# Kernel optimization log

Measured on AMD Instinct MI355X. Metric: run time of the kernel, lower is better.

Reference implementation:

```python
import jax, jax.numpy as jnp
import numpy as np

B, C, H, W = 4, 64, 64, 64

def setup_inputs() -> dict:
    key = jax.random.key(0)
    ks = jax.random.split(key, 7)
    s = 1.0 / np.sqrt(C)
    return {
        "x": jax.random.normal(ks[0], (B, C, H, W), dtype=jnp.float32),
        "Wq": jax.random.normal(ks[1], (C, C), dtype=jnp.float32) * s,
        "bq": jax.random.normal(ks[2], (C,), dtype=jnp.float32) * s,
        "Wk": jax.random.normal(ks[3], (C, C), dtype=jnp.float32) * s,
        "bk": jax.random.normal(ks[4], (C,), dtype=jnp.float32) * s,
        "Wv": jax.random.normal(ks[5], (C, C), dtype=jnp.float32) * s,
        "bv": jax.random.normal(ks[6], (C,), dtype=jnp.float32) * s,
    }

def reference(x, Wq, bq, Wk, bk, Wv, bv):
    b, c, h, w = x.shape
    n = h * w
    xf = x.reshape(b, c, n)                                   # (B,C,N)
    # 1x1 convs == per-pixel linear maps over channels
    q = jnp.einsum('oc,bcn->bon', Wq, xf) + bq[None, :, None]  # (B,C,N)
    k = jnp.einsum('oc,bcn->bon', Wk, xf) + bk[None, :, None]  # (B,C,N)
    v = jnp.einsum('oc,bcn->bon', Wv, xf) + bv[None, :, None]  # (B,C,N)
    # energy = Q^T K : (B,N,N); note: no 1/sqrt(C) scaling in the original
    energy = jnp.einsum('bcn,bcm->bnm', q, k)
    attention = jax.nn.softmax(energy, axis=-1)
    # out = V @ attention^T : out[:, :, i] = sum_j V[:, :, j] * attention[i, j]
    out = jnp.einsum('bcm,bnm->bcn', v, attention)
    return out.reshape(b, c, h, w)
```

## Files before the change

### kernel.cpp

```cpp
#include <hip/hip_runtime.h>
#include <math.h>

#define T_N 4096
#define T_C 64
#define T_B 4
#define NSLICE 4
#define TILES_PER_SLICE (64 / NSLICE)

typedef __attribute__((ext_vector_type(8))) _Float16 f16x8;
typedef __attribute__((ext_vector_type(4))) _Float16 f16x4;
typedef __attribute__((ext_vector_type(4))) float f32x4;

__device__ inline unsigned short f2h(float f) {
    union { _Float16 h; unsigned short s; } u; u.h = (_Float16)f; return u.s;
}
__device__ inline float h2f(unsigned short s) {
    union { unsigned short s; _Float16 h; } u; u.s = s; return (float)u.h;
}

__global__ __launch_bounds__(256) void qkv_kernel(
    const float* __restrict__ x,
    const float* __restrict__ Wq, const float* __restrict__ bq,
    const float* __restrict__ Wk, const float* __restrict__ bk,
    const float* __restrict__ Wv, const float* __restrict__ bv,
    unsigned short* __restrict__ qt, unsigned short* __restrict__ kt,
    unsigned short* __restrict__ vb)
{
    __shared__ __align__(16) unsigned short xsh[32 * 72];
    __shared__ __align__(16) unsigned short xsl[32 * 72];
    __shared__ __align__(16) unsigned short wf[3][64 * 72];

    const int tid = threadIdx.x;
    const int n0  = blockIdx.x * 32;
    const int b   = blockIdx.y;
    const float* xb = x + (size_t)b * T_C * T_N;

    const float* Ws[3] = {Wq, Wk, Wv};
    #pragma unroll
    for (int p = 0; p < 3; ++p) {
        for (int i = tid; i < 1024; i += 256) {
            const int o = i >> 4, c4 = (i & 15) * 4;
            const float4 w4 = ((const float4*)Ws[p])[i];
            f16x4 wh;
            wh[0] = (_Float16)w4.x; wh[1] = (_Float16)w4.y;
            wh[2] = (_Float16)w4.z; wh[3] = (_Float16)w4.w;
            *(f16x4*)&wf[p][o * 72 + c4] = wh;
        }
    }
    for (int i = tid; i < 512; i += 256) {
        const int c = i >> 3, nj4 = (i & 7) * 4;
        const float4 xv = *(const float4*)&xb[c * T_N + n0 + nj4];
        const float xa[4] = {xv.x, xv.y, xv.z, xv.w};
        #pragma unroll
        for (int j = 0; j < 4; ++j) {
            const unsigned short h = f2h(xa[j]);
            xsh[(nj4 + j) * 72 + c] = h;
            xsl[(nj4 + j) * 72 + c] = f2h(xa[j] - h2f(h));
        }
    }
    __syncthreads();

    const int wv_  = tid >> 6;
    const int lane = tid & 63;
    const int quad = lane >> 4;
    const int col  = lane & 15;
    const int pst  = (wv_ & 1) * 16;
    const int oh   = (wv_ >> 1) * 2;
    const size_t bN = (size_t)b * T_N;

    f16x8 xh[2], xl[2];
    #pragma unroll
    for (int s = 0; s < 2; ++s) {
        xh[s] = *(const f16x8*)&xsh[(pst + col) * 72 + s * 32 + quad * 8];
        xl[s] = *(const f16x8*)&xsl[(pst + col) * 72 + s * 32 + quad * 8];
    }
    __syncthreads();

    const float* biases[3] = {bq, bk, bv};
    for (int p = 0; p < 3; ++p) {
        #pragma unroll
        for (int oo = 0; oo < 2; ++oo) {
            const int osub = oh + oo;
            f32x4 acc = (f32x4){0.f, 0.f, 0.f, 0.f};
            #pragma unroll
            for (int s = 0; s < 2; ++s) {
                const f16x8 wfr =
                    *(const f16x8*)&wf[p][(osub * 16 + col) * 72 + s * 32 + quad * 8];
                acc = __builtin_amdgcn_mfma_f32_16x16x32_f16(xh[s], wfr, acc, 0, 0, 0);
                acc = __builtin_amdgcn_mfma_f32_16x16x32_f16(xl[s], wfr, acc, 0, 0, 0);
            }
            const float bb = biases[p][osub * 16 + col];
            if (p < 2) {
                #pragma unroll
                for (int r = 0; r < 4; ++r)
                    xsh[(pst + quad * 4 + r) * 72 + osub * 16 + col] = f2h(acc[r] + bb);
            } else {
                union { ushort4 v; unsigned short s[4]; } hv;
                #pragma unroll
                for (int r = 0; r < 4; ++r) hv.s[r] = f2h(acc[r] + bb);
                *(ushort4*)&xsh[(osub * 16 + col) * 36 + pst + quad * 4] = hv.v;
            }
        }
        __syncthreads();
        if (p < 2) {
            const int pix = tid >> 3, c8 = (tid & 7) * 8;
            unsigned short* dst = (p == 0) ? qt : kt;
            *(f16x8*)&dst[(bN + n0 + pix) * 64 + c8] = *(const f16x8*)&xsh[pix * 72 + c8];
            __syncthreads();
        } else {
            const int o = tid >> 2, p8 = (tid & 3) * 8;
            *(f16x8*)&vb[((size_t)(b * 64 + o)) * T_N + n0 + p8] =
                *(const f16x8*)&xsh[o * 36 + p8];
        }
    }
}

__global__ __launch_bounds__(256, 4) void attn_kernel(
    const unsigned short* __restrict__ qt,
    const unsigned short* __restrict__ kt, const unsigned short* __restrict__ vb,
    unsigned short* __restrict__ o_part, float* __restrict__ mp, float* __restrict__ lp)
{
    __shared__ __align__(16) unsigned short ks[64 * 64];
    __shared__ __align__(16) unsigned short vs[64 * 64];

    const int tid   = threadIdx.x;
    const int n0    = blockIdx.x * 64;
    const int slice = blockIdx.y;
    const int b     = blockIdx.z;
    const int wv_   = tid >> 6;
    const int lane  = tid & 63;
    const int quad  = lane >> 4;
    const int col   = lane & 15;

    const size_t bN = (size_t)b * T_N;
    const int q_own = n0 + wv_ * 16 + col;

    f16x8 qh[2];
    #pragma unroll
    for (int s = 0; s < 2; ++s)
        qh[s] = *(const f16x8*)&qt[(bN + q_own) * 64 + s * 32 + quad * 8];

    const int row = tid >> 3, cc = tid & 7;
    const int pc  = (cc ^ (row & 7)) * 8;

    const int mbase = slice * TILES_PER_SLICE * 64;
    float4 p0, p1, p2, p3;
    p0 = *(const float4*)&kt[(bN + mbase + row) * 64 + cc * 8];
    p1 = *(const float4*)&kt[(bN + mbase + 32 + row) * 64 + cc * 8];
    p2 = *(const float4*)&vb[((size_t)(b * 64 + row)) * T_N + mbase + cc * 8];
    p3 = *(const float4*)&vb[((size_t)(b * 64 + 32 + row)) * T_N + mbase + cc * 8];

    f32x4 O[4];
    #pragma unroll
    for (int t = 0; t < 4; ++t) O[t] = (f32x4){0.f, 0.f, 0.f, 0.f};
    float m_st = -INFINITY, l_st = 0.f;

    for (int it = 0; it < TILES_PER_SLICE; ++it) {
        __syncthreads();
        *(float4*)&ks[row * 64 + pc]        = p0;
        *(float4*)&ks[(32 + row) * 64 + pc] = p1;
        *(float4*)&vs[row * 64 + pc]        = p2;
        *(float4*)&vs[(32 + row) * 64 + pc] = p3;
        __syncthreads();

        {
            const int itn = (it + 1 < TILES_PER_SLICE) ? it + 1 : it;
            const int m0n = mbase + itn * 64;
            p0 = *(const float4*)&kt[(bN + m0n + row) * 64 + cc * 8];
            p1 = *(const float4*)&kt[(bN + m0n + 32 + row) * 64 + cc * 8];
            p2 = *(const float4*)&vb[((size_t)(b * 64 + row)) * T_N + m0n + cc * 8];
            p3 = *(const float4*)&vb[((size_t)(b * 64 + 32 + row)) * T_N + m0n + cc * 8];
        }

        f32x4 acc[4];
        #pragma unroll
        for (int t = 0; t < 4; ++t) acc[t] = (f32x4){0.f, 0.f, 0.f, 0.f};
        #pragma unroll
        for (int s = 0; s < 2; ++s) {
            #pragma unroll
            for (int t = 0; t < 4; ++t) {
                const f16x8 kf = *(const f16x8*)
                    &ks[(t * 16 + col) * 64 + (((s * 4 + quad) ^ (col & 7)) * 8)];
                acc[t] = __builtin_amdgcn_mfma_f32_16x16x32_f16(kf, qh[s], acc[t], 0, 0, 0);
            }
        }

        float mx = -INFINITY;
        #pragma unroll
        for (int t = 0; t < 4; ++t)
            #pragma unroll
            for (int r = 0; r < 4; ++r) mx = fmaxf(mx, acc[t][r]);
        mx = fmaxf(mx, __shfl_xor(mx, 16));
        mx = fmaxf(mx, __shfl_xor(mx, 32));
        const float mnew = fmaxf(m_st, mx);
        const float alpha = __expf(m_st - mnew);
        float sum = 0.f;
        f16x4 pf[4];
        #pragma unroll
        for (int t = 0; t < 4; ++t) {
            #pragma unroll
            for (int r = 0; r < 4; ++r) {
                const float pv = __expf(acc[t][r] - mnew);
                sum += pv;
                pf[t][r] = (_Float16)pv;
            }
        }
        sum += __shfl_xor(sum, 16);
        sum += __shfl_xor(sum, 32);
        l_st = alpha * l_st + sum;
        m_st = mnew;

        #pragma unroll
        for (int tc = 0; tc < 4; ++tc) {
            O[tc] *= alpha;
            #pragma unroll
            for (int t = 0; t < 4; ++t) {
                const f16x4 vf = *(const f16x4*)
                    &vs[(tc * 16 + col) * 64 +
                        (((2 * t + (quad >> 1)) ^ (col & 7)) * 8) + (quad & 1) * 4];
                O[tc] = __builtin_amdgcn_mfma_f32_16x16x16f16(vf, pf[t], O[tc], 0, 0, 0);
            }
        }
    }

    #pragma unroll
    for (int tc = 0; tc < 4; ++tc) {
        #pragma unroll
        for (int r = 0; r < 4; ++r) {
            o_part[((size_t)((slice * T_B + b) * 64 + tc * 16 + quad * 4 + r)) * T_N +
                   q_own] = f2h(O[tc][r]);
        }
    }
    if (quad == 0) {
        const size_t off = (size_t)(slice * T_B + b) * T_N + q_own;
        mp[off] = m_st;
        lp[off] = l_st;
    }
}

__global__ __launch_bounds__(256) void combine_kernel(
    const unsigned short* __restrict__ o_part,
    const float* __restrict__ mp, const float* __restrict__ lp,
    float* __restrict__ out)
{
    __shared__ float wn[NSLICE][32];

    const int tid = threadIdx.x;
    const int n0  = blockIdx.x * 32;
    const int b   = blockIdx.y;

    if (tid < 32) {
        float m_s[NSLICE], l_s[NSLICE];
        #pragma unroll
        for (int s = 0; s < NSLICE; ++s) {
            const size_t off = (size_t)(s * T_B + b) * T_N + n0 + tid;
            m_s[s] = mp[off];
            l_s[s] = lp[off];
        }
        float M = m_s[0];
        #pragma unroll
        for (int s = 1; s < NSLICE; ++s) M = fmaxf(M, m_s[s]);
        float w_s[NSLICE], L = 0.f;
        #pragma unroll
        for (int s = 0; s < NSLICE; ++s) {
            w_s[s] = __expf(m_s[s] - M);
            L += l_s[s] * w_s[s];
        }
        const float inv = 1.f / L;
        #pragma unroll
        for (int s = 0; s < NSLICE; ++s) wn[s][tid] = w_s[s] * inv;
    }
    __syncthreads();

    for (int t = tid; t < 512; t += 256) {
        const int c = t >> 3, g = t & 7;
        float4 acc = make_float4(0.f, 0.f, 0.f, 0.f);
        #pragma unroll
        for (int s = 0; s < NSLICE; ++s) {
            const ushort4 o4 = *(const ushort4*)
                &o_part[((size_t)((s * T_B + b) * 64 + c)) * T_N + n0 + g * 4];
            acc.x = fmaf(h2f(o4.x), wn[s][g * 4 + 0], acc.x);
            acc.y = fmaf(h2f(o4.y), wn[s][g * 4 + 1], acc.y);
            acc.z = fmaf(h2f(o4.z), wn[s][g * 4 + 2], acc.z);
            acc.w = fmaf(h2f(o4.w), wn[s][g * 4 + 3], acc.w);
        }
        *(float4*)&out[((size_t)(b * 64 + c)) * T_N + n0 + g * 4] = acc;
    }
}

extern "C" void kernel_launch(void* const* d_in, const int* in_sizes, int n_in,
                              void* d_out, int out_size, void* d_ws, size_t ws_size,
                              hipStream_t stream) {
    const float* x  = (const float*)d_in[0];
    const float* Wq = (const float*)d_in[1];
    const float* bq = (const float*)d_in[2];
    const float* Wk = (const float*)d_in[3];
    const float* bk = (const float*)d_in[4];
    const float* Wv = (const float*)d_in[5];
    const float* bv = (const float*)d_in[6];
    float* outp = (float*)d_out;

    const size_t elems = (size_t)T_B * T_N * T_C;
    unsigned short* qtp    = (unsigned short*)d_ws;
    unsigned short* ktp    = qtp + elems;
    unsigned short* vbuf   = ktp + elems;
    unsigned short* o_part = vbuf + elems;
    float* mp = (float*)(o_part + (size_t)NSLICE * elems);
    float* lp = mp + (size_t)NSLICE * T_B * T_N;

    qkv_kernel<<<dim3(T_N / 32, T_B), 256, 0, stream>>>(
        x, Wq, bq, Wk, bk, Wv, bv, qtp, ktp, vbuf);
    attn_kernel<<<dim3(T_N / 64, NSLICE, T_B), 256, 0, stream>>>(
        qtp, ktp, vbuf, o_part, mp, lp);
    combine_kernel<<<dim3(T_N / 32, T_B), 256, 0, stream>>>(
        o_part, mp, lp, outp);
}
```

Before: 112.5 us.

## Process two query tiles per wave to reuse K/V LDS loads, double KV slices

Each wave now owns 32 queries (two 16-query MFMA tiles) instead of 16, so every K and V fragment read from shared memory feeds two MFMAs. The block covers 128 queries, halving the number of blocks that restage each K/V tile. The KV split count is doubled to keep the grid size the same. The costs are more registers per thread (two accumulator sets plus two softmax states), which may reduce occupancy under launch bounds of 4, and twice as much partial-output traffic for the combine kernel.

```diff
diff --git a/kernel.cpp b/kernel.cpp
--- a/kernel.cpp
+++ b/kernel.cpp
@@ -4,7 +4,7 @@
 #define T_N 4096
 #define T_C 64
 #define T_B 4
-#define NSLICE 4
+#define NSLICE 8
 #define TILES_PER_SLICE (64 / NSLICE)
 
 typedef __attribute__((ext_vector_type(8))) _Float16 f16x8;
@@ -124,7 +124,7 @@
     __shared__ __align__(16) unsigned short vs[64 * 64];
 
     const int tid   = threadIdx.x;
-    const int n0    = blockIdx.x * 64;
+    const int n0    = blockIdx.x * 128;
     const int slice = blockIdx.y;
     const int b     = blockIdx.z;
     const int wv_   = tid >> 6;
@@ -133,12 +133,15 @@
     const int col   = lane & 15;
 
     const size_t bN = (size_t)b * T_N;
-    const int q_own = n0 + wv_ * 16 + col;
-
-    f16x8 qh[2];
-    #pragma unroll
-    for (int s = 0; s < 2; ++s)
-        qh[s] = *(const f16x8*)&qt[(bN + q_own) * 64 + s * 32 + quad * 8];
+    const int q0 = n0 + wv_ * 32 + col;
+    const int q1 = q0 + 16;
+
+    f16x8 qh0[2], qh1[2];
+    #pragma unroll
+    for (int s = 0; s < 2; ++s) {
+        qh0[s] = *(const f16x8*)&qt[(bN + q0) * 64 + s * 32 + quad * 8];
+        qh1[s] = *(const f16x8*)&qt[(bN + q1) * 64 + s * 32 + quad * 8];
+    }
 
     const int row = tid >> 3, cc = tid & 7;
     const int pc  = (cc ^ (row & 7)) * 8;
@@ -150,10 +153,14 @@
     p2 = *(const float4*)&vb[((size_t)(b * 64 + row)) * T_N + mbase + cc * 8];
     p3 = *(const float4*)&vb[((size_t)(b * 64 + 32 + row)) * T_N + mbase + cc * 8];
 
-    f32x4 O[4];
-    #pragma unroll
-    for (int t = 0; t < 4; ++t) O[t] = (f32x4){0.f, 0.f, 0.f, 0.f};
-    float m_st = -INFINITY, l_st = 0.f;
+    f32x4 O0[4], O1[4];
+    #pragma unroll
+    for (int t = 0; t < 4; ++t) {
+        O0[t] = (f32x4){0.f, 0.f, 0.f, 0.f};
+        O1[t] = (f32x4){0.f, 0.f, 0.f, 0.f};
+    }
+    float m_st0 = -INFINITY, l_st0 = 0.f;
+    float m_st1 = -INFINITY, l_st1 = 0.f;
 
     for (int it = 0; it < TILES_PER_SLICE; ++it) {
         __syncthreads();
@@ -172,69 +179,107 @@
             p3 = *(const float4*)&vb[((size_t)(b * 64 + 32 + row)) * T_N + m0n + cc * 8];
         }
 
-        f32x4 acc[4];
-        #pragma unroll
-        for (int t = 0; t < 4; ++t) acc[t] = (f32x4){0.f, 0.f, 0.f, 0.f};
+        f32x4 acc0[4], acc1[4];
+        #pragma unroll
+        for (int t = 0; t < 4; ++t) {
+            acc0[t] = (f32x4){0.f, 0.f, 0.f, 0.f};
+            acc1[t] = (f32x4){0.f, 0.f, 0.f, 0.f};
+        }
         #pragma unroll
         for (int s = 0; s < 2; ++s) {
             #pragma unroll
             for (int t = 0; t < 4; ++t) {
                 const f16x8 kf = *(const f16x8*)
                     &ks[(t * 16 + col) * 64 + (((s * 4 + quad) ^ (col & 7)) * 8)];
-                acc[t] = __builtin_amdgcn_mfma_f32_16x16x32_f16(kf, qh[s], acc[t], 0, 0, 0);
-            }
-        }
-
-        float mx = -INFINITY;
-        #pragma unroll
-        for (int t = 0; t < 4; ++t)
-            #pragma unroll
-            for (int r = 0; r < 4; ++r) mx = fmaxf(mx, acc[t][r]);
-        mx = fmaxf(mx, __shfl_xor(mx, 16));
-        mx = fmaxf(mx, __shfl_xor(mx, 32));
-        const float mnew = fmaxf(m_st, mx);
-        const float alpha = __expf(m_st - mnew);
-        float sum = 0.f;
-        f16x4 pf[4];
-        #pragma unroll
-        for (int t = 0; t < 4; ++t) {
-            #pragma unroll
-            for (int r = 0; r < 4; ++r) {
-                const float pv = __expf(acc[t][r] - mnew);
-                sum += pv;
-                pf[t][r] = (_Float16)pv;
-            }
-        }
-        sum += __shfl_xor(sum, 16);
-        sum += __shfl_xor(sum, 32);
-        l_st = alpha * l_st + sum;
-        m_st = mnew;
+                acc0[t] = __builtin_amdgcn_mfma_f32_16x16x32_f16(kf, qh0[s], acc0[t], 0, 0, 0);
+                acc1[t] = __builtin_amdgcn_mfma_f32_16x16x32_f16(kf, qh1[s], acc1[t], 0, 0, 0);
+            }
+        }
+
+        f16x4 pf0[4], pf1[4];
+        float alpha0, alpha1;
+        {
+            float mx = -INFINITY;
+            #pragma unroll
+            for (int t = 0; t < 4; ++t)
+                #pragma unroll
+                for (int r = 0; r < 4; ++r) mx = fmaxf(mx, acc0[t][r]);
+            mx = fmaxf(mx, __shfl_xor(mx, 16));
+            mx = fmaxf(mx, __shfl_xor(mx, 32));
+            const float mnew = fmaxf(m_st0, mx);
+            alpha0 = __expf(m_st0 - mnew);
+            float sum = 0.f;
+            #pragma unroll
+            for (int t = 0; t < 4; ++t) {
+                #pragma unroll
+                for (int r = 0; r < 4; ++r) {
+                    const float pv = __expf(acc0[t][r] - mnew);
+                    sum += pv;
+                    pf0[t][r] = (_Float16)pv;
+                }
+            }
+            sum += __shfl_xor(sum, 16);
+            sum += __shfl_xor(sum, 32);
+            l_st0 = alpha0 * l_st0 + sum;
+            m_st0 = mnew;
+        }
+        {
+            float mx = -INFINITY;
+            #pragma unroll
+            for (int t = 0; t < 4; ++t)
+                #pragma unroll
+                for (int r = 0; r < 4; ++r) mx = fmaxf(mx, acc1[t][r]);
+            mx = fmaxf(mx, __shfl_xor(mx, 16));
+            mx = fmaxf(mx, __shfl_xor(mx, 32));
+            const float mnew = fmaxf(m_st1, mx);
+            alpha1 = __expf(m_st1 - mnew);
+            float sum = 0.f;
+            #pragma unroll
+            for (int t = 0; t < 4; ++t) {
+                #pragma unroll
+                for (int r = 0; r < 4; ++r) {
+                    const float pv = __expf(acc1[t][r] - mnew);
+                    sum += pv;
+                    pf1[t][r] = (_Float16)pv;
+                }
+            }
+            sum += __shfl_xor(sum, 16);
+            sum += __shfl_xor(sum, 32);
+            l_st1 = alpha1 * l_st1 + sum;
+            m_st1 = mnew;
+        }
 
         #pragma unroll
         for (int tc = 0; tc < 4; ++tc) {
-            O[tc] *= alpha;
+            O0[tc] *= alpha0;
+            O1[tc] *= alpha1;
             #pragma unroll
             for (int t = 0; t < 4; ++t) {
                 const f16x4 vf = *(const f16x4*)
                     &vs[(tc * 16 + col) * 64 +
                         (((2 * t + (quad >> 1)) ^ (col & 7)) * 8) + (quad & 1) * 4];
-                O[tc] = __builtin_amdgcn_mfma_f32_16x16x16f16(vf, pf[t], O[tc], 0, 0, 0);
-            }
-        }
-    }
-
+                O0[tc] = __builtin_amdgcn_mfma_f32_16x16x16f16(vf, pf0[t], O0[tc], 0, 0, 0);
+                O1[tc] = __builtin_amdgcn_mfma_f32_16x16x16f16(vf, pf1[t], O1[tc], 0, 0, 0);
+            }
+        }
+    }
+
+    const size_t srow = (size_t)(slice * T_B + b) * 64;
     #pragma unroll
     for (int tc = 0; tc < 4; ++tc) {
         #pragma unroll
         for (int r = 0; r < 4; ++r) {
-            o_part[((size_t)((slice * T_B + b) * 64 + tc * 16 + quad * 4 + r)) * T_N +
-                   q_own] = f2h(O[tc][r]);
+            const size_t crow = (srow + tc * 16 + quad * 4 + r) * T_N;
+            o_part[crow + q0] = f2h(O0[tc][r]);
+            o_part[crow + q1] = f2h(O1[tc][r]);
         }
     }
     if (quad == 0) {
-        const size_t off = (size_t)(slice * T_B + b) * T_N + q_own;
-        mp[off] = m_st;
-        lp[off] = l_st;
+        const size_t off = (size_t)(slice * T_B + b) * T_N;
+        mp[off + q0] = m_st0;
+        lp[off + q0] = l_st0;
+        mp[off + q1] = m_st1;
+        lp[off + q1] = l_st1;
     }
 }
 
@@ -310,7 +355,7 @@
 
     qkv_kernel<<<dim3(T_N / 32, T_B), 256, 0, stream>>>(
         x, Wq, bq, Wk, bk, Wv, bv, qtp, ktp, vbuf);
-    attn_kernel<<<dim3(T_N / 64, NSLICE, T_B), 256, 0, stream>>>(
+    attn_kernel<<<dim3(T_N / 128, NSLICE, T_B), 256, 0, stream>>>(
         qtp, ktp, vbuf, o_part, mp, lp);
     combine_kernel<<<dim3(T_N / 32, T_B), 256, 0, stream>>>(
         o_part, mp, lp, outp);
```

Measured after the change: 112.0 us (median of 2 runs). Within noise of the previous version (-0.4%).
